# Performance work log

Hardware: AMD Instinct MI355X
Metric: run time of the kernel (lower is better)

Reference implementation:

```python
import jax, jax.numpy as jnp
import numpy as np
from math import factorial

# ---- static config mirroring Cace.__init__ ----
MAX_L = 3            # max angular degree
N_RBF = 8            # Bessel radial basis size
RB = 8               # n_radial_basis (radial embedding dim after transform)
K = 3                # n_atom_basis -> edge channels C = K*K
NZ = 4               # len(zs)
CUTOFF = 5.5
N_NODES = 2000
N_EDGES = 50000
T_MP = 1             # num_message_passing
MP_NORM = 1.0 / np.sqrt(25.0)   # 1/sqrt(avg_num_neighbors)
C = K * K

def _lxlylz(max_l):
    out = []
    for l in range(max_l + 1):
        for lx in range(l, -1, -1):
            for ly in range(l - lx, -1, -1):
                out.append((lx, ly, l - lx - ly))
    return out

L_LIST = _lxlylz(MAX_L)                 # 20 Cartesian monomials for max_l=3
NL = len(L_LIST)
LX = np.array([t[0] for t in L_LIST]); LY = np.array([t[1] for t in L_LIST]); LZ = np.array([t[2] for t in L_LIST])
DEGS = LX + LY + LZ                     # degree l of each monomial
MULTI = np.array([factorial(int(d)) / (factorial(int(a)) * factorial(int(b)) * factorial(int(c)))
                  for a, b, c, d in zip(LX, LY, LZ, DEGS)], dtype=np.float32)
SEL = np.zeros((NL, MAX_L + 1), np.float32)
SEL[np.arange(NL), DEGS] = 1.0          # monomial -> degree one-hot (for per-l sums)
NB = 1 + (MAX_L + 1)                    # symmetrizer feats: nu=1 (l=0) + nu=2 per l

def bessel(r):  # [E] -> [E, N_RBF]
    n = jnp.arange(1, N_RBF + 1, dtype=r.dtype)
    return jnp.sqrt(2.0 / CUTOFF) * jnp.sin(n[None, :] * jnp.pi * r[:, None] / CUTOFF) / r[:, None]

def poly_cutoff(r):  # MACE-style polynomial cutoff, p=6
    p = 6.0
    u = r / CUTOFF
    f = 1.0 - (p + 1.0) * (p + 2.0) / 2.0 * u**6 + p * (p + 2.0) * u**7 - p * (p + 1.0) / 2.0 * u**8
    return f * (u < 1.0)

def axis_pows(x):  # [E] -> [E, MAX_L+1] = x^0..x^MAX_L (safe grads, handles negatives)
    pows = [jnp.ones_like(x)]
    for _ in range(MAX_L):
        pows.append(pows[-1] * x)
    return jnp.stack(pows, axis=1)

def angular(u):  # unit vectors [E,3] -> Cartesian monomials [E, NL]
    return axis_pows(u[:, 0])[:, LX] * axis_pows(u[:, 1])[:, LY] * axis_pows(u[:, 2])[:, LZ]

def radial_transform(x, W):  # x [N,R,L,C], W [MAX_L+1,R,Rb] shared per degree l
    return jnp.einsum('nrlc,lrb->nblc', x, W[DEGS])

def symmetrize(A):  # A [N,Rb,NL,C] -> B [N,Rb,NB,C]
    b1 = A[:, :, :1, :]  # nu=1: the (0,0,0) monomial (index 0)
    w = (A * A) * jnp.asarray(MULTI)[None, None, :, None]
    b2 = jnp.einsum('nrlc,lm->nrmc', w, jnp.asarray(SEL))  # nu=2 invariant per degree l
    return jnp.concatenate([b1, b2], axis=2)


def setup_inputs() -> dict:
    key = jax.random.key(0)
    ks = jax.random.split(key, 9)
    positions = jax.random.uniform(ks[0], (N_NODES, 3), dtype=jnp.float32) * 12.0
    species = jax.random.randint(ks[1], (N_NODES,), 0, NZ)
    send = jax.random.randint(ks[2], (N_EDGES,), 0, N_NODES)
    off = jax.random.randint(ks[3], (N_EDGES,), 1, N_NODES)
    recv = (send + off) % N_NODES  # no self-edges -> strictly positive edge lengths
    edge_index = jnp.stack([send, recv])
    shifts = jnp.zeros((N_EDGES, 3), jnp.float32)
    W_embed = jax.random.normal(ks[4], (NZ, K), jnp.float32)
    W_radial = jax.random.normal(ks[5], (MAX_L + 1, N_RBF, RB), jnp.float32) / np.sqrt(N_RBF)
    W_mem = jax.random.normal(ks[6], (MAX_L + 1, RB, RB), jnp.float32) / np.sqrt(RB)
    W_ar = jax.random.normal(ks[7], (N_RBF, RB), jnp.float32) / np.sqrt(N_RBF)
    W_chi = jax.random.normal(ks[8], (RB, NB), jnp.float32) * 0.1
    return {"positions": positions, "shifts": shifts, "W_embed": W_embed, "W_radial": W_radial,
            "W_mem": W_mem, "W_ar": W_ar, "W_chi": W_chi, "species": species, "edge_index": edge_index}


def reference(positions, shifts, W_embed, W_radial, W_mem, W_ar, W_chi, species, edge_index):
    n_nodes = positions.shape[0]
    send, recv = edge_index[0], edge_index[1]
    # edge geometry
    vec = positions[recv] - positions[send] + shifts
    lengths = jnp.linalg.norm(vec, axis=-1)
    u = vec / (lengths[:, None] + 1e-9)
    rad = bessel(lengths)          # [E,R]
    fcut = poly_cutoff(lengths)    # [E]
    ang = angular(u)               # [E,NL]
    # edge type encoding: outer product of sender/receiver species embeddings
    emb = W_embed[species]         # [N,K]
    enc = (emb[send][:, :, None] * emb[recv][:, None, :]).reshape(-1, C)  # [E,C]
    # elementwise_multiply_3tensors -> [E,R,NL,C]
    edge_attri = jnp.einsum('er,el,ec->erlc', rad * fcut[:, None], ang, enc)
    A = radial_transform(jax.ops.segment_sum(edge_attri, recv, num_segments=n_nodes), W_radial)  # [N,Rb,NL,C]
    B = symmetrize(A)              # [N,Rb,NB,C]
    feats = [B]
    for _ in range(T_MP):
        mem = jnp.einsum('nrlc,lrb->nblc', A, W_mem[DEGS])        # NodeMemory
        chi = jnp.einsum('nbkc,bk->nc', B, W_chi)                  # MessageBchi node scalar
        msg_bchi = edge_attri * chi[send][:, None, None, :]
        A_bchi = radial_transform(jax.ops.segment_sum(msg_bchi, recv, num_segments=n_nodes), W_radial)
        fr = (rad @ W_ar) * fcut[:, None]                          # MessageAr radial filter [E,Rb]
        msg_ar = A[send] * fr[:, :, None, None]
        A_ar = jax.ops.segment_sum(msg_ar, recv, num_segments=n_nodes)
        A = (A_ar + A_bchi) * MP_NORM + mem
        B = symmetrize(A)
        feats.append(B)
    return jnp.stack(feats, axis=-1)   # [N,Rb,NB,C,T_MP+1]
```

## Files before the change

kernel.cpp:

```cpp
#include <hip/hip_runtime.h>
#include <hip/hip_bf16.h>


#define CUTF 5.5f
#define MPNORM 0.2f

__constant__ int   d_DEGS[20]  = {0,1,1,1,2,2,2,2,2,2,3,3,3,3,3,3,3,3,3,3};
__constant__ float d_MULTI[20] = {1,1,1,1,1,2,2,1,2,1,1,3,3,3,6,3,1,3,3,1};

__global__ void k_count(const int* __restrict__ eidx, int* __restrict__ counts, int E) {
  int e = blockIdx.x * blockDim.x + threadIdx.x;
  if (e < E) atomicAdd(&counts[eidx[E + e]], 1);
}

__global__ void k_scan(const int* __restrict__ counts, int* __restrict__ offs, int N) {
  __shared__ int part[256];
  int t = threadIdx.x;
  int local[8]; int sum = 0;
  #pragma unroll
  for (int i = 0; i < 8; i++) {
    int idx = t*8 + i;
    int v = (idx < N) ? counts[idx] : 0;
    local[i] = sum; sum += v;
  }
  part[t] = sum; __syncthreads();
  for (int d = 1; d < 256; d <<= 1) {
    int add = (t >= d) ? part[t-d] : 0;
    __syncthreads();
    part[t] += add;
    __syncthreads();
  }
  int excl = part[t] - sum;
  #pragma unroll
  for (int i = 0; i < 8; i++) {
    int idx = t*8 + i;
    if (idx < N) offs[idx] = excl + local[i];
  }
  if (t == 255) offs[N] = part[255];
}

__global__ void k_edge(const float* __restrict__ pos,
                       const float* __restrict__ shifts,
                       const float* __restrict__ Wemb,
                       const float* __restrict__ War,
                       const int* __restrict__ species,
                       const int* __restrict__ eidx,
                       const int* __restrict__ offs,
                       int* __restrict__ cursor,
                       float* __restrict__ edata,
                       int* __restrict__ esend,
                       int E) {
  __shared__ float war_s[64];
  int t = threadIdx.x;
  if (t < 64) war_s[t] = War[t];
  __syncthreads();
  int e = blockIdx.x * blockDim.x + t;
  if (e >= E) return;
  int s  = eidx[e];
  int rI = eidx[E + e];
  float vx = pos[rI*3+0] - pos[s*3+0] + shifts[e*3+0];
  float vy = pos[rI*3+1] - pos[s*3+1] + shifts[e*3+1];
  float vz = pos[rI*3+2] - pos[s*3+2] + shifts[e*3+2];
  float len = sqrtf(vx*vx + vy*vy + vz*vz);
  float inv = 1.0f / (len + 1e-9f);
  float ux = vx*inv, uy = vy*inv, uz = vz*inv;
  float uu = len * (1.0f/CUTF);
  float u2 = uu*uu, u6 = u2*u2*u2;
  float fcut = (uu < 1.0f) ? (1.0f - 28.0f*u6 + 48.0f*u6*uu - 21.0f*u6*u2) : 0.0f;
  float x = 3.14159265358979f * uu;
  float sn = sinf(x), c2 = 2.0f*cosf(x), snm1 = 0.0f;
  float pref = sqrtf(2.0f/CUTF) / (len + 1e-20f);
  float rad[8];
  float v[48];
  #pragma unroll
  for (int k = 0; k < 8; k++) {
    rad[k] = pref * sn;
    v[k]   = rad[k] * fcut;
    float nxt = c2*sn - snm1; snm1 = sn; sn = nxt;
  }
  #pragma unroll
  for (int b = 0; b < 8; b++) {
    float a = 0.0f;
    #pragma unroll
    for (int k = 0; k < 8; k++) a += rad[k] * war_s[k*8+b];
    v[8+b] = a * fcut;
  }
  float px2 = ux*ux, py2 = uy*uy, pz2 = uz*uz;
  v[16] = 1.0f; v[17] = ux;     v[18] = uy;     v[19] = uz;
  v[20] = px2;  v[21] = ux*uy;  v[22] = ux*uz;  v[23] = py2;
  v[24] = uy*uz;v[25] = pz2;
  v[26] = px2*ux; v[27] = px2*uy; v[28] = px2*uz; v[29] = ux*py2;
  v[30] = ux*uy*uz; v[31] = ux*pz2; v[32] = py2*uy; v[33] = py2*uz;
  v[34] = uy*pz2; v[35] = pz2*uz;
  int zs = species[s], zr = species[rI];
  float es0 = Wemb[zs*3+0], es1 = Wemb[zs*3+1], es2 = Wemb[zs*3+2];
  float er0 = Wemb[zr*3+0], er1 = Wemb[zr*3+1], er2 = Wemb[zr*3+2];
  v[36] = es0*er0; v[37] = es0*er1; v[38] = es0*er2;
  v[39] = es1*er0; v[40] = es1*er1; v[41] = es1*er2;
  v[42] = es2*er0; v[43] = es2*er1; v[44] = es2*er2;
  v[45] = 0.0f; v[46] = 0.0f; v[47] = 0.0f;
  int slot = atomicAdd(&cursor[rI], 1);
  int dst = offs[rI] + slot;
  float4* eb4 = reinterpret_cast<float4*>(edata + (size_t)dst * 48);
  #pragma unroll
  for (int w = 0; w < 12; w++)
    eb4[w] = make_float4(v[4*w], v[4*w+1], v[4*w+2], v[4*w+3]);
  esend[dst] = s;
}

__global__ __launch_bounds__(192) void k_nodeA(
    const float* __restrict__ edata, const int* __restrict__ offs,
    const float* __restrict__ Wrad, const float* __restrict__ Wchi,
    float* __restrict__ A, unsigned int* __restrict__ Abf2,
    float* __restrict__ chi, float* __restrict__ B0, int N) {
  __shared__ float wr_s[288];
  __shared__ float wchi_s[40];
  __shared__ float Bsh[360];
  int t = threadIdx.x, n = blockIdx.x;
  for (int i = t; i < 256; i += 192) { int d = i >> 6, rm = i & 63; wr_s[d*72+rm] = Wrad[i]; }
  for (int i = t; i < 40;  i += 192) wchi_s[i] = Wchi[i];
  for (int i = t; i < 360; i += 192) Bsh[i] = 0.0f;
  int l = t / 9, c = t - l*9;
  bool act = t < 180;
  int ll = act ? l : 0, cc = act ? c : 0;
  float acc[8];
  #pragma unroll
  for (int r = 0; r < 8; r++) acc[r] = 0.0f;
  int start = offs[n], end = offs[n+1];
  #pragma unroll 4
  for (int j = start; j < end; j++) {
    const float* row = edata + (size_t)j * 48;
    float p = row[16+ll] * row[36+cc];
    #pragma unroll
    for (int r = 0; r < 8; r++) acc[r] += row[r] * p;
  }
  __syncthreads();
  int deg = act ? d_DEGS[ll] : 0;
  const float* wp = &wr_s[deg*72];
  float Ab[8];
  #pragma unroll
  for (int b = 0; b < 8; b++) {
    float a = 0.0f;
    #pragma unroll
    for (int r = 0; r < 8; r++) a += acc[r] * wp[r*8+b];
    Ab[b] = a;
  }
  if (act) {
    #pragma unroll
    for (int b = 0; b < 8; b++) A[(size_t)n*1440 + t*8 + b] = Ab[b];
    #pragma unroll
    for (int bp = 0; bp < 4; bp++) {
      __hip_bfloat16 blo = __float2bfloat16(Ab[2*bp]);
      __hip_bfloat16 bhi = __float2bfloat16(Ab[2*bp+1]);
      unsigned int pr = (unsigned int)(*reinterpret_cast<unsigned short*>(&blo))
                      | ((unsigned int)(*reinterpret_cast<unsigned short*>(&bhi)) << 16);
      Abf2[(size_t)bp*N*180 + (size_t)n*180 + t] = pr;
    }
    if (l == 0) {
      #pragma unroll
      for (int b = 0; b < 8; b++) Bsh[b*45 + c] = Ab[b];
    }
    float mlt = d_MULTI[ll]; int kk = 1 + deg;
    #pragma unroll
    for (int b = 0; b < 8; b++) atomicAdd(&Bsh[b*45 + kk*9 + c], mlt*Ab[b]*Ab[b]);
  }
  __syncthreads();
  if (t < 9) {
    float s = 0.0f;
    for (int b = 0; b < 8; b++)
      #pragma unroll
      for (int kq = 0; kq < 5; kq++) s += Bsh[b*45 + kq*9 + t] * wchi_s[b*5 + kq];
    chi[n*9 + t] = s;
  }
  for (int i = t; i < 360; i += 192)
    B0[(size_t)n*360 + i] = Bsh[i];
}

__global__ __launch_bounds__(192) void k_node2(
    const float* __restrict__ edata, const int* __restrict__ esend,
    const int* __restrict__ offs,
    const float* __restrict__ Wrad, const float* __restrict__ Wmem,
    const float* __restrict__ A, const unsigned int* __restrict__ Abf2,
    const float* __restrict__ chi, const float* __restrict__ B0,
    float* __restrict__ out, int N) {
  __shared__ float wr_s[288], wm_s[288];
  __shared__ float Bsh[360];
  int t = threadIdx.x, n = blockIdx.x;
  for (int i = t; i < 256; i += 192) {
    int d = i >> 6, rm = i & 63;
    wr_s[d*72+rm] = Wrad[i];
    wm_s[d*72+rm] = Wmem[i];
  }
  for (int i = t; i < 360; i += 192) Bsh[i] = 0.0f;
  int l = t / 9, c = t - l*9;
  bool act = t < 180;
  int ll = act ? l : 0, cc = act ? c : 0;
  int tt = act ? t : 0;
  size_t plane = (size_t)N * 180;
  float Sacc[8], ARacc[8];
  #pragma unroll
  for (int r = 0; r < 8; r++) { Sacc[r] = 0.0f; ARacc[r] = 0.0f; }
  int start = offs[n], end = offs[n+1];
  #pragma unroll 4
  for (int j = start; j < end; j++) {
    const float* row = edata + (size_t)j * 48;
    int snd = esend[j];
    float ch = chi[snd*9 + cc];
    float pch = row[16+ll] * row[36+cc] * ch;
    #pragma unroll
    for (int r = 0; r < 8; r++) Sacc[r] += row[r] * pch;
    const unsigned int* gp = Abf2 + (size_t)snd*180 + tt;
    unsigned int q0 = gp[0];
    unsigned int q1 = gp[plane];
    unsigned int q2 = gp[2*plane];
    unsigned int q3 = gp[3*plane];
    float a0 = __uint_as_float(q0 << 16), a1 = __uint_as_float(q0 & 0xffff0000u);
    float a2 = __uint_as_float(q1 << 16), a3 = __uint_as_float(q1 & 0xffff0000u);
    float a4 = __uint_as_float(q2 << 16), a5 = __uint_as_float(q2 & 0xffff0000u);
    float a6 = __uint_as_float(q3 << 16), a7 = __uint_as_float(q3 & 0xffff0000u);
    ARacc[0] += a0*row[8];  ARacc[1] += a1*row[9];
    ARacc[2] += a2*row[10]; ARacc[3] += a3*row[11];
    ARacc[4] += a4*row[12]; ARacc[5] += a5*row[13];
    ARacc[6] += a6*row[14]; ARacc[7] += a7*row[15];
  }
  __syncthreads();
  if (act) {
    int deg = d_DEGS[ll];
    const float* wrp = &wr_s[deg*72];
    const float* wmp = &wm_s[deg*72];
    const float* aop = A + (size_t)n*1440 + t*8;
    float aown[8];
    #pragma unroll
    for (int r = 0; r < 8; r++) aown[r] = aop[r];
    float newA[8];
    #pragma unroll
    for (int b = 0; b < 8; b++) {
      float mem = 0.0f, ab = 0.0f;
      #pragma unroll
      for (int r = 0; r < 8; r++) { mem += aown[r]*wmp[r*8+b]; ab += Sacc[r]*wrp[r*8+b]; }
      newA[b] = (ARacc[b] + ab)*MPNORM + mem;
    }
    if (l == 0) {
      #pragma unroll
      for (int b = 0; b < 8; b++) Bsh[b*45 + c] = newA[b];
    }
    float mlt = d_MULTI[ll]; int kk = 1 + deg;
    #pragma unroll
    for (int b = 0; b < 8; b++) atomicAdd(&Bsh[b*45 + kk*9 + c], mlt*newA[b]*newA[b]);
  }
  __syncthreads();
  float2* out2 = reinterpret_cast<float2*>(out);
  for (int i = t; i < 360; i += 192) {
    float2 pk; pk.x = B0[(size_t)n*360 + i]; pk.y = Bsh[i];
    out2[(size_t)n*360 + i] = pk;
  }
}

extern "C" void kernel_launch(void* const* d_in, const int* in_sizes, int n_in,
                              void* d_out, int out_size, void* d_ws, size_t ws_size,
                              hipStream_t stream) {
  const float* pos    = (const float*)d_in[0];
  const float* shifts = (const float*)d_in[1];
  const float* Wemb   = (const float*)d_in[2];
  const float* Wrad   = (const float*)d_in[3];
  const float* Wmem   = (const float*)d_in[4];
  const float* War    = (const float*)d_in[5];
  const float* Wchi   = (const float*)d_in[6];
  const int* species = (const int*)d_in[7];
  const int* eidx    = (const int*)d_in[8];
  float* out = (float*)d_out;
  int N = in_sizes[7];
  int E = in_sizes[8] / 2;

  char* base = (char*)d_ws;
  size_t off = 0;
  float* edata = (float*)(base + off); off += (size_t)E*48*4;
  float* A     = (float*)(base + off); off += (size_t)N*1440*4;
  unsigned int* Abf2 = (unsigned int*)(base + off); off += (size_t)N*180*4*4;
  float* chi   = (float*)(base + off); off += (size_t)N*9*4;
  float* B0    = (float*)(base + off); off += (size_t)N*360*4;
  int* counts  = (int*)(base + off);   off += (size_t)N*4;
  int* cursor  = (int*)(base + off);   off += (size_t)N*4;
  int* offs    = (int*)(base + off);   off += (((size_t)(N+1)*4) + 15) & ~(size_t)15;
  int* esend   = (int*)(base + off);   off += (size_t)E*4;

  hipMemsetAsync(counts, 0, (size_t)N*2*4, stream);
  int eb = (E + 255) / 256;
  k_count<<<eb, 256, 0, stream>>>(eidx, counts, E);
  k_scan<<<1, 256, 0, stream>>>(counts, offs, N);
  k_edge<<<eb, 256, 0, stream>>>(pos, shifts, Wemb, War, species, eidx, offs, cursor,
                                 edata, esend, E);
  k_nodeA<<<N, 192, 0, stream>>>(edata, offs, Wrad, Wchi, A, Abf2, chi, B0, N);
  k_node2<<<N, 192, 0, stream>>>(edata, esend, offs, Wrad, Wmem, A, Abf2, chi, B0, out, N);
}
```

Baseline: 169.0 us.

## Pre-apply radial weight per degree on edges and stage edge tiles in LDS

The per-degree radial transform W_radial is moved from the node side onto each edge: the edge kernel now stores four pre-transformed 8-wide radial vectors (one per degree), so node kernels accumulate directly in the output basis and skip the post-sum 8x8 matvec. The node kernels also copy edge rows in tiles of 48 into shared memory with cooperative float4 loads instead of every thread reading global rows. This widens each edge record from 48 to 80 floats, raising edge-data write and read traffic, and adds extra block barriers per tile.

Result: slower. 177.4 us (+4.9%).

```diff
diff --git a/kernel.cpp b/kernel.cpp
--- a/kernel.cpp
+++ b/kernel.cpp
@@ -4,6 +4,7 @@
 
 #define CUTF 5.5f
 #define MPNORM 0.2f
+#define TILE 48
 
 __constant__ int   d_DEGS[20]  = {0,1,1,1,2,2,2,2,2,2,3,3,3,3,3,3,3,3,3,3};
 __constant__ float d_MULTI[20] = {1,1,1,1,1,2,2,1,2,1,1,3,3,3,6,3,1,3,3,1};
@@ -42,6 +43,7 @@
 __global__ void k_edge(const float* __restrict__ pos,
                        const float* __restrict__ shifts,
                        const float* __restrict__ Wemb,
+                       const float* __restrict__ Wrad,
                        const float* __restrict__ War,
                        const int* __restrict__ species,
                        const int* __restrict__ eidx,
@@ -51,8 +53,10 @@
                        int* __restrict__ esend,
                        int E) {
   __shared__ float war_s[64];
+  __shared__ float wrad_s[256];
   int t = threadIdx.x;
   if (t < 64) war_s[t] = War[t];
+  wrad_s[t] = Wrad[t];
   __syncthreads();
   int e = blockIdx.x * blockDim.x + t;
   if (e >= E) return;
@@ -70,81 +74,91 @@
   float x = 3.14159265358979f * uu;
   float sn = sinf(x), c2 = 2.0f*cosf(x), snm1 = 0.0f;
   float pref = sqrtf(2.0f/CUTF) / (len + 1e-20f);
-  float rad[8];
-  float v[48];
+  float rad[8], g[8];
   #pragma unroll
   for (int k = 0; k < 8; k++) {
     rad[k] = pref * sn;
-    v[k]   = rad[k] * fcut;
+    g[k]   = rad[k] * fcut;
     float nxt = c2*sn - snm1; snm1 = sn; sn = nxt;
   }
+  float v[80];
+  #pragma unroll
+  for (int d = 0; d < 4; d++)
+    #pragma unroll
+    for (int b = 0; b < 8; b++) {
+      float a = 0.0f;
+      #pragma unroll
+      for (int r = 0; r < 8; r++) a += g[r] * wrad_s[d*64 + r*8 + b];
+      v[d*8+b] = a;
+    }
   #pragma unroll
   for (int b = 0; b < 8; b++) {
     float a = 0.0f;
     #pragma unroll
     for (int k = 0; k < 8; k++) a += rad[k] * war_s[k*8+b];
-    v[8+b] = a * fcut;
+    v[32+b] = a * fcut;
   }
   float px2 = ux*ux, py2 = uy*uy, pz2 = uz*uz;
-  v[16] = 1.0f; v[17] = ux;     v[18] = uy;     v[19] = uz;
-  v[20] = px2;  v[21] = ux*uy;  v[22] = ux*uz;  v[23] = py2;
-  v[24] = uy*uz;v[25] = pz2;
-  v[26] = px2*ux; v[27] = px2*uy; v[28] = px2*uz; v[29] = ux*py2;
-  v[30] = ux*uy*uz; v[31] = ux*pz2; v[32] = py2*uy; v[33] = py2*uz;
-  v[34] = uy*pz2; v[35] = pz2*uz;
+  v[40] = 1.0f; v[41] = ux;     v[42] = uy;     v[43] = uz;
+  v[44] = px2;  v[45] = ux*uy;  v[46] = ux*uz;  v[47] = py2;
+  v[48] = uy*uz;v[49] = pz2;
+  v[50] = px2*ux; v[51] = px2*uy; v[52] = px2*uz; v[53] = ux*py2;
+  v[54] = ux*uy*uz; v[55] = ux*pz2; v[56] = py2*uy; v[57] = py2*uz;
+  v[58] = uy*pz2; v[59] = pz2*uz;
   int zs = species[s], zr = species[rI];
   float es0 = Wemb[zs*3+0], es1 = Wemb[zs*3+1], es2 = Wemb[zs*3+2];
   float er0 = Wemb[zr*3+0], er1 = Wemb[zr*3+1], er2 = Wemb[zr*3+2];
-  v[36] = es0*er0; v[37] = es0*er1; v[38] = es0*er2;
-  v[39] = es1*er0; v[40] = es1*er1; v[41] = es1*er2;
-  v[42] = es2*er0; v[43] = es2*er1; v[44] = es2*er2;
-  v[45] = 0.0f; v[46] = 0.0f; v[47] = 0.0f;
+  v[60] = es0*er0; v[61] = es0*er1; v[62] = es0*er2;
+  v[63] = es1*er0; v[64] = es1*er1; v[65] = es1*er2;
+  v[66] = es2*er0; v[67] = es2*er1; v[68] = es2*er2;
+  #pragma unroll
+  for (int w = 69; w < 80; w++) v[w] = 0.0f;
   int slot = atomicAdd(&cursor[rI], 1);
   int dst = offs[rI] + slot;
-  float4* eb4 = reinterpret_cast<float4*>(edata + (size_t)dst * 48);
-  #pragma unroll
-  for (int w = 0; w < 12; w++)
+  float4* eb4 = reinterpret_cast<float4*>(edata + (size_t)dst * 80);
+  #pragma unroll
+  for (int w = 0; w < 20; w++)
     eb4[w] = make_float4(v[4*w], v[4*w+1], v[4*w+2], v[4*w+3]);
   esend[dst] = s;
 }
 
 __global__ __launch_bounds__(192) void k_nodeA(
     const float* __restrict__ edata, const int* __restrict__ offs,
-    const float* __restrict__ Wrad, const float* __restrict__ Wchi,
+    const float* __restrict__ Wchi,
     float* __restrict__ A, unsigned int* __restrict__ Abf2,
     float* __restrict__ chi, float* __restrict__ B0, int N) {
-  __shared__ float wr_s[288];
   __shared__ float wchi_s[40];
   __shared__ float Bsh[360];
+  __shared__ __align__(16) float est[TILE*80];
   int t = threadIdx.x, n = blockIdx.x;
-  for (int i = t; i < 256; i += 192) { int d = i >> 6, rm = i & 63; wr_s[d*72+rm] = Wrad[i]; }
   for (int i = t; i < 40;  i += 192) wchi_s[i] = Wchi[i];
   for (int i = t; i < 360; i += 192) Bsh[i] = 0.0f;
   int l = t / 9, c = t - l*9;
   bool act = t < 180;
   int ll = act ? l : 0, cc = act ? c : 0;
-  float acc[8];
-  #pragma unroll
-  for (int r = 0; r < 8; r++) acc[r] = 0.0f;
+  int deg = act ? d_DEGS[ll] : 0;
+  float Ab[8];
+  #pragma unroll
+  for (int b = 0; b < 8; b++) Ab[b] = 0.0f;
   int start = offs[n], end = offs[n+1];
-  #pragma unroll 4
-  for (int j = start; j < end; j++) {
-    const float* row = edata + (size_t)j * 48;
-    float p = row[16+ll] * row[36+cc];
-    #pragma unroll
-    for (int r = 0; r < 8; r++) acc[r] += row[r] * p;
-  }
-  __syncthreads();
-  int deg = act ? d_DEGS[ll] : 0;
-  const float* wp = &wr_s[deg*72];
-  float Ab[8];
-  #pragma unroll
-  for (int b = 0; b < 8; b++) {
-    float a = 0.0f;
-    #pragma unroll
-    for (int r = 0; r < 8; r++) a += acc[r] * wp[r*8+b];
-    Ab[b] = a;
-  }
+  for (int tb = start; tb < end; tb += TILE) {
+    int cnt = min(TILE, end - tb);
+    __syncthreads();
+    const float4* src = reinterpret_cast<const float4*>(edata + (size_t)tb*80);
+    float4* dst = reinterpret_cast<float4*>(est);
+    for (int i = t; i < cnt*20; i += 192) dst[i] = src[i];
+    __syncthreads();
+    #pragma unroll 4
+    for (int j = 0; j < cnt; j++) {
+      const float* eb = est + j*80;
+      float p = eb[40+ll] * eb[60+cc];
+      const float4* gw4 = reinterpret_cast<const float4*>(eb + deg*8);
+      float4 g0 = gw4[0], g1 = gw4[1];
+      Ab[0] += p*g0.x; Ab[1] += p*g0.y; Ab[2] += p*g0.z; Ab[3] += p*g0.w;
+      Ab[4] += p*g1.x; Ab[5] += p*g1.y; Ab[6] += p*g1.z; Ab[7] += p*g1.w;
+    }
+  }
+  __syncthreads();
   if (act) {
     #pragma unroll
     for (int b = 0; b < 8; b++) A[(size_t)n*1440 + t*8 + b] = Ab[b];
@@ -178,55 +192,64 @@
 
 __global__ __launch_bounds__(192) void k_node2(
     const float* __restrict__ edata, const int* __restrict__ esend,
-    const int* __restrict__ offs,
-    const float* __restrict__ Wrad, const float* __restrict__ Wmem,
+    const int* __restrict__ offs, const float* __restrict__ Wmem,
     const float* __restrict__ A, const unsigned int* __restrict__ Abf2,
     const float* __restrict__ chi, const float* __restrict__ B0,
     float* __restrict__ out, int N) {
-  __shared__ float wr_s[288], wm_s[288];
+  __shared__ float wm_s[288];
   __shared__ float Bsh[360];
+  __shared__ int   snd_s[TILE];
+  __shared__ __align__(16) float est[TILE*80];
   int t = threadIdx.x, n = blockIdx.x;
-  for (int i = t; i < 256; i += 192) {
-    int d = i >> 6, rm = i & 63;
-    wr_s[d*72+rm] = Wrad[i];
-    wm_s[d*72+rm] = Wmem[i];
-  }
+  for (int i = t; i < 256; i += 192) { int d = i >> 6, rm = i & 63; wm_s[d*72+rm] = Wmem[i]; }
   for (int i = t; i < 360; i += 192) Bsh[i] = 0.0f;
   int l = t / 9, c = t - l*9;
   bool act = t < 180;
   int ll = act ? l : 0, cc = act ? c : 0;
   int tt = act ? t : 0;
+  int deg = act ? d_DEGS[ll] : 0;
   size_t plane = (size_t)N * 180;
-  float Sacc[8], ARacc[8];
-  #pragma unroll
-  for (int r = 0; r < 8; r++) { Sacc[r] = 0.0f; ARacc[r] = 0.0f; }
+  float Sb[8], ARacc[8];
+  #pragma unroll
+  for (int b = 0; b < 8; b++) { Sb[b] = 0.0f; ARacc[b] = 0.0f; }
   int start = offs[n], end = offs[n+1];
-  #pragma unroll 4
-  for (int j = start; j < end; j++) {
-    const float* row = edata + (size_t)j * 48;
-    int snd = esend[j];
-    float ch = chi[snd*9 + cc];
-    float pch = row[16+ll] * row[36+cc] * ch;
-    #pragma unroll
-    for (int r = 0; r < 8; r++) Sacc[r] += row[r] * pch;
-    const unsigned int* gp = Abf2 + (size_t)snd*180 + tt;
-    unsigned int q0 = gp[0];
-    unsigned int q1 = gp[plane];
-    unsigned int q2 = gp[2*plane];
-    unsigned int q3 = gp[3*plane];
-    float a0 = __uint_as_float(q0 << 16), a1 = __uint_as_float(q0 & 0xffff0000u);
-    float a2 = __uint_as_float(q1 << 16), a3 = __uint_as_float(q1 & 0xffff0000u);
-    float a4 = __uint_as_float(q2 << 16), a5 = __uint_as_float(q2 & 0xffff0000u);
-    float a6 = __uint_as_float(q3 << 16), a7 = __uint_as_float(q3 & 0xffff0000u);
-    ARacc[0] += a0*row[8];  ARacc[1] += a1*row[9];
-    ARacc[2] += a2*row[10]; ARacc[3] += a3*row[11];
-    ARacc[4] += a4*row[12]; ARacc[5] += a5*row[13];
-    ARacc[6] += a6*row[14]; ARacc[7] += a7*row[15];
+  for (int tb = start; tb < end; tb += TILE) {
+    int cnt = min(TILE, end - tb);
+    __syncthreads();
+    const float4* src = reinterpret_cast<const float4*>(edata + (size_t)tb*80);
+    float4* dst = reinterpret_cast<float4*>(est);
+    for (int i = t; i < cnt*20; i += 192) dst[i] = src[i];
+    for (int i = t; i < cnt; i += 192) snd_s[i] = esend[tb + i];
+    __syncthreads();
+    #pragma unroll 4
+    for (int j = 0; j < cnt; j++) {
+      const float* eb = est + j*80;
+      int snd = snd_s[j];
+      float ch = chi[snd*9 + cc];
+      float pch = eb[40+ll] * eb[60+cc] * ch;
+      const float4* gw4 = reinterpret_cast<const float4*>(eb + deg*8);
+      float4 g0 = gw4[0], g1 = gw4[1];
+      Sb[0] += pch*g0.x; Sb[1] += pch*g0.y; Sb[2] += pch*g0.z; Sb[3] += pch*g0.w;
+      Sb[4] += pch*g1.x; Sb[5] += pch*g1.y; Sb[6] += pch*g1.z; Sb[7] += pch*g1.w;
+      const float4* fr4 = reinterpret_cast<const float4*>(eb + 32);
+      float4 f0 = fr4[0], f1 = fr4[1];
+      const unsigned int* gp = Abf2 + (size_t)snd*180 + tt;
+      unsigned int q0 = gp[0];
+      unsigned int q1 = gp[plane];
+      unsigned int q2 = gp[2*plane];
+      unsigned int q3 = gp[3*plane];
+      float a0 = __uint_as_float(q0 << 16), a1 = __uint_as_float(q0 & 0xffff0000u);
+      float a2 = __uint_as_float(q1 << 16), a3 = __uint_as_float(q1 & 0xffff0000u);
+      float a4 = __uint_as_float(q2 << 16), a5 = __uint_as_float(q2 & 0xffff0000u);
+      float a6 = __uint_as_float(q3 << 16), a7 = __uint_as_float(q3 & 0xffff0000u);
+      ARacc[0] += a0*f0.x; ARacc[1] += a1*f0.y;
+      ARacc[2] += a2*f0.z; ARacc[3] += a3*f0.w;
+      ARacc[4] += a4*f1.x; ARacc[5] += a5*f1.y;
+      ARacc[6] += a6*f1.z; ARacc[7] += a7*f1.w;
+    }
   }
   __syncthreads();
   if (act) {
-    int deg = d_DEGS[ll];
-    const float* wrp = &wr_s[deg*72];
     const float* wmp = &wm_s[deg*72];
     const float* aop = A + (size_t)n*1440 + t*8;
     float aown[8];
@@ -235,10 +258,10 @@
     float newA[8];
     #pragma unroll
     for (int b = 0; b < 8; b++) {
-      float mem = 0.0f, ab = 0.0f;
-      #pragma unroll
-      for (int r = 0; r < 8; r++) { mem += aown[r]*wmp[r*8+b]; ab += Sacc[r]*wrp[r*8+b]; }
-      newA[b] = (ARacc[b] + ab)*MPNORM + mem;
+      float mem = 0.0f;
+      #pragma unroll
+      for (int r = 0; r < 8; r++) mem += aown[r]*wmp[r*8+b];
+      newA[b] = (ARacc[b] + Sb[b])*MPNORM + mem;
     }
     if (l == 0) {
       #pragma unroll
@@ -274,7 +297,7 @@
 
   char* base = (char*)d_ws;
   size_t off = 0;
-  float* edata = (float*)(base + off); off += (size_t)E*48*4;
+  float* edata = (float*)(base + off); off += (size_t)E*80*4;
   float* A     = (float*)(base + off); off += (size_t)N*1440*4;
   unsigned int* Abf2 = (unsigned int*)(base + off); off += (size_t)N*180*4*4;
   float* chi   = (float*)(base + off); off += (size_t)N*9*4;
@@ -288,8 +311,8 @@
   int eb = (E + 255) / 256;
   k_count<<<eb, 256, 0, stream>>>(eidx, counts, E);
   k_scan<<<1, 256, 0, stream>>>(counts, offs, N);
-  k_edge<<<eb, 256, 0, stream>>>(pos, shifts, Wemb, War, species, eidx, offs, cursor,
-                                 edata, esend, E);
-  k_nodeA<<<N, 192, 0, stream>>>(edata, offs, Wrad, Wchi, A, Abf2, chi, B0, N);
-  k_node2<<<N, 192, 0, stream>>>(edata, esend, offs, Wrad, Wmem, A, Abf2, chi, B0, out, N);
-}
+  k_edge<<<eb, 256, 0, stream>>>(pos, shifts, Wemb, Wrad, War, species, eidx, offs,
+                                 cursor, edata, esend, E);
+  k_nodeA<<<N, 192, 0, stream>>>(edata, offs, Wchi, A, Abf2, chi, B0, N);
+  k_node2<<<N, 192, 0, stream>>>(edata, esend, offs, Wmem, A, Abf2, chi, B0, out, N);
+}
```
